# Performance work log

Measured on AMD Instinct MI355X. Metric: run time of the kernel, lower is better.

Reference implementation:

```python
import jax, jax.numpy as jnp
import numpy as np

N_EMBD = 1024
D_FF = 4 * N_EMBD
RANK = 4
NUM_LOOPS = 4
SCALE = 1.0 / RANK  # alpha=1.0 / r=4


def setup_inputs() -> dict:
    key = jax.random.key(0)
    ks = jax.random.split(key, 8)
    B, T = 8, 2048
    x = jax.random.normal(ks[0], (B, T, N_EMBD), dtype=jnp.float32)
    # base linears (torch nn.Linear weight layout: [out, in]), bias=False
    W1 = jax.random.normal(ks[1], (D_FF, N_EMBD), dtype=jnp.float32) * (1.0 / np.sqrt(N_EMBD))
    W2 = jax.random.normal(ks[2], (N_EMBD, D_FF), dtype=jnp.float32) * (1.0 / np.sqrt(D_FF))
    # LoRA factors: A [num_loops, r, in], B [num_loops, out, r]
    # (torch inits lora_B to zeros; we use small random values so the LoRA path is exercised)
    A1 = jax.random.normal(ks[3], (NUM_LOOPS, RANK, N_EMBD), dtype=jnp.float32) * (1.0 / np.sqrt(N_EMBD))
    B1 = jax.random.normal(ks[4], (NUM_LOOPS, D_FF, RANK), dtype=jnp.float32) * 0.01
    A2 = jax.random.normal(ks[5], (NUM_LOOPS, RANK, D_FF), dtype=jnp.float32) * (1.0 / np.sqrt(D_FF))
    B2 = jax.random.normal(ks[6], (NUM_LOOPS, N_EMBD, RANK), dtype=jnp.float32) * 0.01
    adapter_id = 1
    return {"x": x, "W1": W1, "A1": A1, "B1": B1, "W2": W2, "A2": A2, "B2": B2,
            "adapter_id": adapter_id}


def _lora_linear(x, W, A, B, adapter_id):
    # base: x @ W.T  (torch F.linear)
    out = jnp.einsum('btd,fd->btf', x, W)
    Aa = A[adapter_id]  # [r, in]
    Ba = B[adapter_id]  # [out, r]
    # low-rank correction: ((x @ A.T) @ B.T) * scale
    delta = jnp.einsum('btr,fr->btf', jnp.einsum('btd,rd->btr', x, Aa), Ba) * SCALE
    return out + delta


def reference(x, W1, A1, B1, W2, A2, B2, adapter_id):
    h = jax.nn.relu(_lora_linear(x, W1, A1, B1, adapter_id))
    out = _lora_linear(h, W2, A2, B2, adapter_id)
    # Dropout in eval mode (identity); see notes.
    return out
```

## Files before the change

kernel.cpp:

```cpp
#include <hip/hip_runtime.h>
#include <stdint.h>

typedef __bf16 bf16;
typedef __attribute__((ext_vector_type(8))) __bf16 bf16x8;
typedef __attribute__((ext_vector_type(4))) float f32x4;

#define LORA_SCALE 0.25f

__device__ __forceinline__ void gload_lds16(const bf16* g, bf16* l) {
    __builtin_amdgcn_global_load_lds(
        (const __attribute__((address_space(1))) uint32_t*)g,
        (__attribute__((address_space(3))) uint32_t*)l,
        16, 0, 0);
}

__device__ __forceinline__ bf16x8 cvt8(const float* p) {
    f32x4 a = *(const f32x4*)p;
    f32x4 b = *(const f32x4*)(p + 4);
    bf16x8 r;
    r[0] = (bf16)a[0]; r[1] = (bf16)a[1]; r[2] = (bf16)a[2]; r[3] = (bf16)a[3];
    r[4] = (bf16)b[0]; r[5] = (bf16)b[1]; r[6] = (bf16)b[2]; r[7] = (bf16)b[3];
    return r;
}

__global__ __launch_bounds__(256)
void cvt_weights(const float* __restrict__ in1, bf16* __restrict__ out1, int n1,
                 const float* __restrict__ in2, bf16* __restrict__ out2, int n2) {
    const int64_t idx = (int64_t)(blockIdx.x * 256 + threadIdx.x) * 8;
    if (idx < n1) *(bf16x8*)&out1[idx] = cvt8(&in1[idx]);
    else          *(bf16x8*)&out2[idx - n1] = cvt8(&in2[idx - n1]);
}

__global__ __launch_bounds__(256)
void lora1(const float* __restrict__ X, const float* __restrict__ Aall,
           const int* __restrict__ adapter, float* __restrict__ T,
           bf16* __restrict__ Xb)
{
    const int K = 1024;
    const int gid = blockIdx.x * 256 + threadIdx.x;
    const int aid = adapter[0];
    const float* Aa = Aall + (int64_t)aid * 4 * K;
    const int wid  = gid >> 6;
    const int lane = threadIdx.x & 63;
    const int m0   = wid * 4;

    float acc[4][4];
    #pragma unroll
    for (int rr = 0; rr < 4; rr++)
        #pragma unroll
        for (int r = 0; r < 4; r++) acc[rr][r] = 0.f;

    #pragma unroll
    for (int it = 0; it < K / 512; it++) {
        const int k = it * 512 + lane * 8;
        float av[4][8];
        #pragma unroll
        for (int r = 0; r < 4; r++) {
            f32x4 a = *(const f32x4*)&Aa[r * K + k];
            f32x4 b = *(const f32x4*)&Aa[r * K + k + 4];
            av[r][0]=a[0]; av[r][1]=a[1]; av[r][2]=a[2]; av[r][3]=a[3];
            av[r][4]=b[0]; av[r][5]=b[1]; av[r][6]=b[2]; av[r][7]=b[3];
        }
        #pragma unroll
        for (int rr = 0; rr < 4; rr++) {
            const float* xp = X + (int64_t)(m0 + rr) * K + k;
            f32x4 a = *(const f32x4*)xp;
            f32x4 b = *(const f32x4*)(xp + 4);
            float xv[8] = {a[0],a[1],a[2],a[3],b[0],b[1],b[2],b[3]};
            bf16x8 xb;
            #pragma unroll
            for (int e = 0; e < 8; e++) xb[e] = (bf16)xv[e];
            *(bf16x8*)&Xb[(int64_t)(m0 + rr) * K + k] = xb;
            #pragma unroll
            for (int r = 0; r < 4; r++)
                #pragma unroll
                for (int e = 0; e < 8; e++)
                    acc[rr][r] += xv[e] * av[r][e];
        }
    }
    #pragma unroll
    for (int rr = 0; rr < 4; rr++)
        #pragma unroll
        for (int r = 0; r < 4; r++)
            #pragma unroll
            for (int off = 32; off >= 1; off >>= 1)
                acc[rr][r] += __shfl_xor(acc[rr][r], off);
    if (lane == 0) {
        #pragma unroll
        for (int rr = 0; rr < 4; rr++) {
            f32x4 t;
            t[0] = acc[rr][0]; t[1] = acc[rr][1]; t[2] = acc[rr][2]; t[3] = acc[rr][3];
            *(f32x4*)&T[(int64_t)(m0 + rr) * 4] = t;
        }
    }
}

__global__ __launch_bounds__(256)
void t2_reduce(const float* __restrict__ T2p, float* __restrict__ T2,
               int M, int NP) {
    const int i = blockIdx.x * 256 + threadIdx.x;
    float s = 0.f;
    for (int p = 0; p < NP; p++) s += T2p[(int64_t)p * M * 4 + i];
    T2[i] = s;
}

template<bool RELU, typename CT, int PART, bool FUSET2>
__global__ __launch_bounds__(256, 2)
void gemm_lora(const bf16* __restrict__ A,
               const bf16* __restrict__ Bm,
               CT* __restrict__ C,
               const float* __restrict__ Tlo,
               const float* __restrict__ Blo,
               const int* __restrict__ adapter,
               const float* __restrict__ A2,
               float* __restrict__ T2p,
               int M, int N, int K)
{
    __shared__ bf16 smem[256 * 64 + 128 * 64];
    bf16* sA = smem;
    bf16* sB = smem + 256 * 64;

    const int tid  = threadIdx.x;
    const int lane = tid & 63;
    const int w    = tid >> 6;
    const int quad = lane >> 4;
    const int l16  = lane & 15;

    int bx, by;
    {
        const int Nt = gridDim.x, Mt = gridDim.y;
        const int id = blockIdx.y * Nt + blockIdx.x;
        const int xcd = id & 7, k = id >> 3;
        if (PART == 0) { const int q = Nt >> 3; bx = xcd * q + (k % q); by = k / q; }
        else           { const int q = Mt >> 3; bx = k % Nt; by = xcd * q + (k / Nt); }
    }
    const int nBase = bx * 128;
    const int mBase = by * 256;
    const int wm = (w >> 1) * 128;
    const int wn = (w & 1) * 64;

    f32x4 acc[8][4];
    #pragma unroll
    for (int i = 0; i < 8; i++)
        #pragma unroll
        for (int j = 0; j < 4; j++)
            #pragma unroll
            for (int e = 0; e < 4; e++)
                acc[i][j][e] = 0.f;

    const bf16* gA = A  + (int64_t)mBase * K;
    const bf16* gB = Bm + (int64_t)nBase * K;
    const int ldRow  = tid >> 3;
    const int swzCol = ((tid & 7) ^ ((tid >> 3) & 7)) * 8;

    for (int kt = 0; kt < K; kt += 64) {
        #pragma unroll
        for (int i = 0; i < 8; i++)
            gload_lds16(gA + (int64_t)(i * 32 + ldRow) * K + kt + swzCol,
                        sA + (i * 32 + w * 8) * 64);
        #pragma unroll
        for (int i = 0; i < 4; i++)
            gload_lds16(gB + (int64_t)(i * 32 + ldRow) * K + kt + swzCol,
                        sB + (i * 32 + w * 8) * 64);
        __syncthreads();
        #pragma unroll
        for (int ks = 0; ks < 2; ks++) {
            const int kpos = (((ks * 4 + quad) ^ (l16 & 7))) * 8;
            bf16x8 af[8], bfv[4];
            #pragma unroll
            for (int i = 0; i < 8; i++)
                af[i] = *(const bf16x8*)&sA[(wm + i * 16 + l16) * 64 + kpos];
            #pragma unroll
            for (int j = 0; j < 4; j++)
                bfv[j] = *(const bf16x8*)&sB[(wn + j * 16 + l16) * 64 + kpos];
            #pragma unroll
            for (int i = 0; i < 8; i++)
                #pragma unroll
                for (int j = 0; j < 4; j++)
                    acc[i][j] = __builtin_amdgcn_mfma_f32_16x16x32_bf16(af[i], bfv[j], acc[i][j], 0, 0, 0);
        }
        __syncthreads();
    }

    const int aid = adapter[0];
    const float* Ba = Blo + (int64_t)aid * N * 4;

    f32x4 bv[4];
    #pragma unroll
    for (int j = 0; j < 4; j++) {
        const int f = nBase + wn + j * 16 + l16;
        bv[j] = *(const f32x4*)&Ba[(int64_t)f * 4];
    }

    float a2v[4][4];
    if (FUSET2) {
        const float* A2a = A2 + (int64_t)aid * 4 * N;
        #pragma unroll
        for (int j = 0; j < 4; j++) {
            const int f = nBase + wn + j * 16 + l16;
            #pragma unroll
            for (int r2 = 0; r2 < 4; r2++)
                a2v[j][r2] = A2a[(int64_t)r2 * N + f];
        }
    }
    float* T2row = FUSET2 ? T2p + ((int64_t)(bx * 2 + (w & 1)) * M) * 4 : nullptr;

    if constexpr (sizeof(CT) == 2) {
        bf16* scratch = smem + w * (64 * 72);
        #pragma unroll
        for (int g = 0; g < 2; g++) {
            #pragma unroll
            for (int mi2 = 0; mi2 < 4; mi2++) {
                const int mi = g * 4 + mi2;
                f32x4 tv[4];
                #pragma unroll
                for (int r = 0; r < 4; r++) {
                    const int m = mBase + wm + mi * 16 + quad * 4 + r;
                    tv[r] = *(const f32x4*)&Tlo[(int64_t)m * 4];
                }
                float tp[4][4];
                if (FUSET2)
                    #pragma unroll
                    for (int r = 0; r < 4; r++)
                        #pragma unroll
                        for (int r2 = 0; r2 < 4; r2++) tp[r][r2] = 0.f;
                #pragma unroll
                for (int j = 0; j < 4; j++) {
                    #pragma unroll
                    for (int r = 0; r < 4; r++) {
                        const float d = tv[r][0] * bv[j][0] + tv[r][1] * bv[j][1]
                                      + tv[r][2] * bv[j][2] + tv[r][3] * bv[j][3];
                        float v = acc[mi][j][r] + LORA_SCALE * d;
                        if (RELU) v = v > 0.f ? v : 0.f;
                        if (FUSET2)
                            #pragma unroll
                            for (int r2 = 0; r2 < 4; r2++)
                                tp[r][r2] += v * a2v[j][r2];
                        scratch[(mi2 * 16 + quad * 4 + r) * 72 + j * 16 + l16] = (bf16)v;
                    }
                }
                if (FUSET2) {
                    #pragma unroll
                    for (int r = 0; r < 4; r++)
                        #pragma unroll
                        for (int r2 = 0; r2 < 4; r2++)
                            #pragma unroll
                            for (int off = 8; off >= 1; off >>= 1)
                                tp[r][r2] += __shfl_xor(tp[r][r2], off);
                    if (l16 == 0) {
                        #pragma unroll
                        for (int r = 0; r < 4; r++) {
                            const int m = mBase + wm + mi * 16 + quad * 4 + r;
                            f32x4 o;
                            o[0] = tp[r][0]; o[1] = tp[r][1];
                            o[2] = tp[r][2]; o[3] = tp[r][3];
                            *(f32x4*)&T2row[(int64_t)m * 4] = o;
                        }
                    }
                }
            }
            #pragma unroll
            for (int p = 0; p < 8; p++) {
                const int row = p * 8 + (lane >> 3);
                bf16x8 vv = *(const bf16x8*)&scratch[row * 72 + (lane & 7) * 8];
                const int m = mBase + wm + g * 64 + row;
                *(bf16x8*)&C[(int64_t)m * N + nBase + wn + (lane & 7) * 8] = vv;
            }
        }
    } else {
        #pragma unroll
        for (int mi = 0; mi < 8; mi++) {
            f32x4 tv[4];
            #pragma unroll
            for (int r = 0; r < 4; r++) {
                const int m = mBase + wm + mi * 16 + quad * 4 + r;
                tv[r] = *(const f32x4*)&Tlo[(int64_t)m * 4];
            }
            #pragma unroll
            for (int j = 0; j < 4; j++) {
                #pragma unroll
                for (int r = 0; r < 4; r++) {
                    const float d = tv[r][0] * bv[j][0] + tv[r][1] * bv[j][1]
                                  + tv[r][2] * bv[j][2] + tv[r][3] * bv[j][3];
                    float v = acc[mi][j][r] + LORA_SCALE * d;
                    if (RELU) v = v > 0.f ? v : 0.f;
                    const int m = mBase + wm + mi * 16 + quad * 4 + r;
                    C[(int64_t)m * N + nBase + wn + j * 16 + l16] = v;
                }
            }
        }
    }
}

extern "C" void kernel_launch(void* const* d_in, const int* in_sizes, int n_in,
                              void* d_out, int out_size, void* d_ws, size_t ws_size,
                              hipStream_t stream) {
    const float* x  = (const float*)d_in[0];
    const float* W1 = (const float*)d_in[1];
    const float* A1 = (const float*)d_in[2];
    const float* B1 = (const float*)d_in[3];
    const float* W2 = (const float*)d_in[4];
    const float* A2 = (const float*)d_in[5];
    const float* B2 = (const float*)d_in[6];
    const int* adapter = (const int*)d_in[7];
    float* out = (float*)d_out;

    const int M = 16384, D = 1024, F = 4096;
    const int Nt1 = F / 128;

    bf16*  h   = (bf16*)d_ws;
    bf16*  xb  = h + (size_t)M * F;
    bf16*  wb1 = xb + (size_t)M * D;
    bf16*  wb2 = wb1 + (size_t)F * D;
    float* t1  = (float*)(wb2 + (size_t)D * F);
    float* t2  = t1 + (size_t)M * 4;
    float* t2p = t2 + (size_t)M * 4;

    lora1<<<M / 16, 256, 0, stream>>>(x, A1, adapter, t1, xb);
    cvt_weights<<<(2 * F * D) / 2048, 256, 0, stream>>>(W1, wb1, F * D, W2, wb2, D * F);
    dim3 g1(Nt1, M / 256);
    gemm_lora<true, bf16, 0, true><<<g1, 256, 0, stream>>>(
        xb, wb1, h, t1, B1, adapter, A2, t2p, M, F, D);
    t2_reduce<<<(M * 4) / 256, 256, 0, stream>>>(t2p, t2, M, 2 * Nt1);
    dim3 g2(D / 128, M / 256);
    gemm_lora<false, float, 1, false><<<g2, 256, 0, stream>>>(
        h, wb2, out, t2, B2, adapter, nullptr, nullptr, M, D, F);
}
```

Baseline: 446.2 us.

## Rewrite LoRA GEMM as 8-wave 256x256 tile with double-buffered LDS pipeline

Replaces the 4-wave 256x128 GEMM with an 8-wave, 512-thread kernel computing 256x256 tiles. K-chunks are split into 32-wide halves and staged into double-buffered LDS with direct global-to-LDS loads issued ahead of use. Explicit vmcnt/lgkmcnt waits, barriers and s_setprio interleave loads with MFMA bursts. The fp32 output path now goes through an LDS scratch so stores are vectorised. This aims to hide memory latency and raise reuse per tile, at the cost of 128KB of LDS (which may limit occupancy to one block per CU) and fragile hand-written wait counts.

```diff
diff --git a/kernel.cpp b/kernel.cpp
--- a/kernel.cpp
+++ b/kernel.cpp
@@ -105,20 +105,18 @@
 }
 
 template<bool RELU, typename CT, int PART, bool FUSET2>
-__global__ __launch_bounds__(256, 2)
-void gemm_lora(const bf16* __restrict__ A,
-               const bf16* __restrict__ Bm,
-               CT* __restrict__ C,
-               const float* __restrict__ Tlo,
-               const float* __restrict__ Blo,
-               const int* __restrict__ adapter,
-               const float* __restrict__ A2,
-               float* __restrict__ T2p,
-               int M, int N, int K)
+__global__ __launch_bounds__(512, 2)
+void gemm_lora8(const bf16* __restrict__ A,
+                const bf16* __restrict__ Bm,
+                CT* __restrict__ C,
+                const float* __restrict__ Tlo,
+                const float* __restrict__ Blo,
+                const int* __restrict__ adapter,
+                const float* __restrict__ A2,
+                float* __restrict__ T2p,
+                int M, int N, int K)
 {
-    __shared__ bf16 smem[256 * 64 + 128 * 64];
-    bf16* sA = smem;
-    bf16* sB = smem + 256 * 64;
+    __shared__ alignas(16) bf16 smem[65536];
 
     const int tid  = threadIdx.x;
     const int lane = tid & 63;
@@ -134,159 +132,249 @@
         if (PART == 0) { const int q = Nt >> 3; bx = xcd * q + (k % q); by = k / q; }
         else           { const int q = Mt >> 3; bx = k % Nt; by = xcd * q + (k / Nt); }
     }
-    const int nBase = bx * 128;
+    const int nBase = bx * 256;
     const int mBase = by * 256;
-    const int wm = (w >> 1) * 128;
-    const int wn = (w & 1) * 64;
-
-    f32x4 acc[8][4];
+    const int wm = (w >> 1) * 64;
+    const int wn = (w & 1) * 128;
+
+    f32x4 acc[4][8];
     #pragma unroll
-    for (int i = 0; i < 8; i++)
-        #pragma unroll
-        for (int j = 0; j < 4; j++)
-            #pragma unroll
-            for (int e = 0; e < 4; e++)
-                acc[i][j][e] = 0.f;
+    for (int i = 0; i < 4; i++)
+        #pragma unroll
+        for (int j = 0; j < 8; j++)
+            #pragma unroll
+            for (int e = 0; e < 4; e++) acc[i][j][e] = 0.f;
 
     const bf16* gA = A  + (int64_t)mBase * K;
     const bf16* gB = Bm + (int64_t)nBase * K;
-    const int ldRow  = tid >> 3;
-    const int swzCol = ((tid & 7) ^ ((tid >> 3) & 7)) * 8;
-
-    for (int kt = 0; kt < K; kt += 64) {
-        #pragma unroll
-        for (int i = 0; i < 8; i++)
-            gload_lds16(gA + (int64_t)(i * 32 + ldRow) * K + kt + swzCol,
-                        sA + (i * 32 + w * 8) * 64);
-        #pragma unroll
-        for (int i = 0; i < 4; i++)
-            gload_lds16(gB + (int64_t)(i * 32 + ldRow) * K + kt + swzCol,
-                        sB + (i * 32 + w * 8) * 64);
-        __syncthreads();
-        #pragma unroll
-        for (int ks = 0; ks < 2; ks++) {
-            const int kpos = (((ks * 4 + quad) ^ (l16 & 7))) * 8;
-            bf16x8 af[8], bfv[4];
-            #pragma unroll
-            for (int i = 0; i < 8; i++)
-                af[i] = *(const bf16x8*)&sA[(wm + i * 16 + l16) * 64 + kpos];
+
+    const int sq    = (tid & 3) ^ ((tid >> 3) & 3);
+    const int srow  = ((tid >> 3) << 1) | ((tid >> 2) & 1);
+    const bf16* sA0 = gA + (int64_t)srow * K + sq * 8;
+    const bf16* sA1 = gA + (int64_t)(srow + 128) * K + sq * 8;
+    const bf16* sB0 = gB + (int64_t)srow * K + sq * 8;
+    const bf16* sB1 = gB + (int64_t)(srow + 128) * K + sq * 8;
+    const int dstW  = w * 512;
+
+    const int pc8  = (quad ^ ((l16 >> 1) & 3)) * 8;
+    const int aOff = (wm + l16) * 32 + pc8;
+    const int bOff = (wn + l16) * 32 + pc8;
+
+    const int NT = K >> 6;
+
+    auto stage = [&](const bf16* s0, const bf16* s1, int t, int uidx) {
+        bf16* u = smem + ((t & 1) * 4 + uidx) * 8192;
+        const int co = t * 64 + (uidx >> 1) * 32;
+        gload_lds16(s0 + co, u + dstW);
+        gload_lds16(s1 + co, u + dstW + 4096);
+    };
+
+    stage(sA0, sA1, 0, 0); stage(sB0, sB1, 0, 1);
+    stage(sA0, sA1, 0, 2); stage(sB0, sB1, 0, 3);
+    if (NT > 1) {
+        asm volatile("s_waitcnt vmcnt(4)" ::: "memory");
+        stage(sA0, sA1, 1, 0); stage(sB0, sB1, 1, 1); stage(sA0, sA1, 1, 2);
+        asm volatile("s_waitcnt vmcnt(6)" ::: "memory");
+    } else {
+        asm volatile("s_waitcnt vmcnt(0)" ::: "memory");
+    }
+    __builtin_amdgcn_s_barrier();
+    __builtin_amdgcn_sched_barrier(0);
+
+    for (int t = 0; t < NT; ++t) {
+        const bf16* u0 = smem + (t & 1) * 32768;
+        const bf16* u1 = u0 + 8192;
+        const bf16* u2 = u0 + 16384;
+        const bf16* u3 = u0 + 24576;
+        const bool sNext  = (t + 1 < NT);
+        const bool sNext2 = (t + 2 < NT);
+
+        bf16x8 a0[4], bA[4];
+        #pragma unroll
+        for (int mi = 0; mi < 4; mi++) a0[mi] = *(const bf16x8*)&u0[aOff + mi * 512];
+        #pragma unroll
+        for (int j = 0; j < 4; j++)   bA[j]  = *(const bf16x8*)&u1[bOff + j * 512];
+        if (sNext) stage(sB0, sB1, t + 1, 3);
+        __builtin_amdgcn_s_barrier();
+        __builtin_amdgcn_sched_barrier(0);
+        asm volatile("s_waitcnt lgkmcnt(0)" ::: "memory");
+        __builtin_amdgcn_s_setprio(1);
+        #pragma unroll
+        for (int mi = 0; mi < 4; mi++)
             #pragma unroll
             for (int j = 0; j < 4; j++)
-                bfv[j] = *(const bf16x8*)&sB[(wn + j * 16 + l16) * 64 + kpos];
-            #pragma unroll
-            for (int i = 0; i < 8; i++)
-                #pragma unroll
-                for (int j = 0; j < 4; j++)
-                    acc[i][j] = __builtin_amdgcn_mfma_f32_16x16x32_bf16(af[i], bfv[j], acc[i][j], 0, 0, 0);
-        }
-        __syncthreads();
+                acc[mi][j] = __builtin_amdgcn_mfma_f32_16x16x32_bf16(a0[mi], bA[j], acc[mi][j], 0, 0, 0);
+        __builtin_amdgcn_s_setprio(0);
+        __builtin_amdgcn_s_barrier();
+        __builtin_amdgcn_sched_barrier(0);
+
+        bf16x8 bB[4];
+        #pragma unroll
+        for (int j = 0; j < 4; j++) bB[j] = *(const bf16x8*)&u1[bOff + (4 + j) * 512];
+        if (sNext2) stage(sA0, sA1, t + 2, 0);
+        __builtin_amdgcn_s_barrier();
+        __builtin_amdgcn_sched_barrier(0);
+        asm volatile("s_waitcnt lgkmcnt(0)" ::: "memory");
+        __builtin_amdgcn_s_setprio(1);
+        #pragma unroll
+        for (int mi = 0; mi < 4; mi++)
+            #pragma unroll
+            for (int j = 0; j < 4; j++)
+                acc[mi][4 + j] = __builtin_amdgcn_mfma_f32_16x16x32_bf16(a0[mi], bB[j], acc[mi][4 + j], 0, 0, 0);
+        __builtin_amdgcn_s_setprio(0);
+        __builtin_amdgcn_s_barrier();
+        __builtin_amdgcn_sched_barrier(0);
+
+        bf16x8 a1[4], bC[4];
+        #pragma unroll
+        for (int mi = 0; mi < 4; mi++) a1[mi] = *(const bf16x8*)&u2[aOff + mi * 512];
+        #pragma unroll
+        for (int j = 0; j < 4; j++)   bC[j]  = *(const bf16x8*)&u3[bOff + j * 512];
+        if (sNext2) stage(sB0, sB1, t + 2, 1);
+        __builtin_amdgcn_s_barrier();
+        __builtin_amdgcn_sched_barrier(0);
+        asm volatile("s_waitcnt lgkmcnt(0)" ::: "memory");
+        __builtin_amdgcn_s_setprio(1);
+        #pragma unroll
+        for (int mi = 0; mi < 4; mi++)
+            #pragma unroll
+            for (int j = 0; j < 4; j++)
+                acc[mi][j] = __builtin_amdgcn_mfma_f32_16x16x32_bf16(a1[mi], bC[j], acc[mi][j], 0, 0, 0);
+        __builtin_amdgcn_s_setprio(0);
+        __builtin_amdgcn_s_barrier();
+        __builtin_amdgcn_sched_barrier(0);
+
+        bf16x8 bD[4];
+        #pragma unroll
+        for (int j = 0; j < 4; j++) bD[j] = *(const bf16x8*)&u3[bOff + (4 + j) * 512];
+        if (sNext2) stage(sA0, sA1, t + 2, 2);
+        __builtin_amdgcn_s_barrier();
+        __builtin_amdgcn_sched_barrier(0);
+        asm volatile("s_waitcnt lgkmcnt(0)" ::: "memory");
+        __builtin_amdgcn_s_setprio(1);
+        #pragma unroll
+        for (int mi = 0; mi < 4; mi++)
+            #pragma unroll
+            for (int j = 0; j < 4; j++)
+                acc[mi][4 + j] = __builtin_amdgcn_mfma_f32_16x16x32_bf16(a1[mi], bD[j], acc[mi][4 + j], 0, 0, 0);
+        __builtin_amdgcn_s_setprio(0);
+        if (sNext) {
+            if (sNext2) asm volatile("s_waitcnt vmcnt(6)" ::: "memory");
+            else        asm volatile("s_waitcnt vmcnt(0)" ::: "memory");
+        }
+        __builtin_amdgcn_s_barrier();
+        __builtin_amdgcn_sched_barrier(0);
     }
 
     const int aid = adapter[0];
     const float* Ba = Blo + (int64_t)aid * N * 4;
 
-    f32x4 bv[4];
+    f32x4 bv[8];
     #pragma unroll
-    for (int j = 0; j < 4; j++) {
+    for (int j = 0; j < 8; j++) {
         const int f = nBase + wn + j * 16 + l16;
         bv[j] = *(const f32x4*)&Ba[(int64_t)f * 4];
     }
 
-    float a2v[4][4];
-    if (FUSET2) {
+    float a2v[8][4];
+    if constexpr (FUSET2) {
         const float* A2a = A2 + (int64_t)aid * 4 * N;
         #pragma unroll
-        for (int j = 0; j < 4; j++) {
+        for (int j = 0; j < 8; j++) {
             const int f = nBase + wn + j * 16 + l16;
             #pragma unroll
             for (int r2 = 0; r2 < 4; r2++)
                 a2v[j][r2] = A2a[(int64_t)r2 * N + f];
         }
     }
-    float* T2row = FUSET2 ? T2p + ((int64_t)(bx * 2 + (w & 1)) * M) * 4 : nullptr;
+    float* T2row = FUSET2 ? T2p + (int64_t)(bx * 2 + (w & 1)) * M * 4 : nullptr;
 
     if constexpr (sizeof(CT) == 2) {
-        bf16* scratch = smem + w * (64 * 72);
-        #pragma unroll
-        for (int g = 0; g < 2; g++) {
-            #pragma unroll
-            for (int mi2 = 0; mi2 < 4; mi2++) {
-                const int mi = g * 4 + mi2;
-                f32x4 tv[4];
-                #pragma unroll
-                for (int r = 0; r < 4; r++) {
-                    const int m = mBase + wm + mi * 16 + quad * 4 + r;
-                    tv[r] = *(const f32x4*)&Tlo[(int64_t)m * 4];
-                }
-                float tp[4][4];
-                if (FUSET2)
-                    #pragma unroll
-                    for (int r = 0; r < 4; r++)
-                        #pragma unroll
-                        for (int r2 = 0; r2 < 4; r2++) tp[r][r2] = 0.f;
-                #pragma unroll
-                for (int j = 0; j < 4; j++) {
-                    #pragma unroll
-                    for (int r = 0; r < 4; r++) {
-                        const float d = tv[r][0] * bv[j][0] + tv[r][1] * bv[j][1]
-                                      + tv[r][2] * bv[j][2] + tv[r][3] * bv[j][3];
-                        float v = acc[mi][j][r] + LORA_SCALE * d;
-                        if (RELU) v = v > 0.f ? v : 0.f;
-                        if (FUSET2)
-                            #pragma unroll
-                            for (int r2 = 0; r2 < 4; r2++)
-                                tp[r][r2] += v * a2v[j][r2];
-                        scratch[(mi2 * 16 + quad * 4 + r) * 72 + j * 16 + l16] = (bf16)v;
-                    }
-                }
-                if (FUSET2) {
-                    #pragma unroll
-                    for (int r = 0; r < 4; r++)
-                        #pragma unroll
-                        for (int r2 = 0; r2 < 4; r2++)
-                            #pragma unroll
-                            for (int off = 8; off >= 1; off >>= 1)
-                                tp[r][r2] += __shfl_xor(tp[r][r2], off);
-                    if (l16 == 0) {
-                        #pragma unroll
-                        for (int r = 0; r < 4; r++) {
-                            const int m = mBase + wm + mi * 16 + quad * 4 + r;
-                            f32x4 o;
-                            o[0] = tp[r][0]; o[1] = tp[r][1];
-                            o[2] = tp[r][2]; o[3] = tp[r][3];
-                            *(f32x4*)&T2row[(int64_t)m * 4] = o;
-                        }
-                    }
-                }
-            }
-            #pragma unroll
-            for (int p = 0; p < 8; p++) {
-                const int row = p * 8 + (lane >> 3);
-                bf16x8 vv = *(const bf16x8*)&scratch[row * 72 + (lane & 7) * 8];
-                const int m = mBase + wm + g * 64 + row;
-                *(bf16x8*)&C[(int64_t)m * N + nBase + wn + (lane & 7) * 8] = vv;
-            }
-        }
-    } else {
-        #pragma unroll
-        for (int mi = 0; mi < 8; mi++) {
+        bf16* scratch = smem + w * (16 * 136);
+        #pragma unroll
+        for (int mi = 0; mi < 4; mi++) {
             f32x4 tv[4];
             #pragma unroll
             for (int r = 0; r < 4; r++) {
                 const int m = mBase + wm + mi * 16 + quad * 4 + r;
                 tv[r] = *(const f32x4*)&Tlo[(int64_t)m * 4];
             }
-            #pragma unroll
-            for (int j = 0; j < 4; j++) {
+            float tp[4][4];
+            if constexpr (FUSET2)
+                #pragma unroll
+                for (int r = 0; r < 4; r++)
+                    #pragma unroll
+                    for (int r2 = 0; r2 < 4; r2++) tp[r][r2] = 0.f;
+            #pragma unroll
+            for (int j = 0; j < 8; j++) {
                 #pragma unroll
                 for (int r = 0; r < 4; r++) {
                     const float d = tv[r][0] * bv[j][0] + tv[r][1] * bv[j][1]
                                   + tv[r][2] * bv[j][2] + tv[r][3] * bv[j][3];
                     float v = acc[mi][j][r] + LORA_SCALE * d;
                     if (RELU) v = v > 0.f ? v : 0.f;
-                    const int m = mBase + wm + mi * 16 + quad * 4 + r;
-                    C[(int64_t)m * N + nBase + wn + j * 16 + l16] = v;
+                    if constexpr (FUSET2)
+                        #pragma unroll
+                        for (int r2 = 0; r2 < 4; r2++) tp[r][r2] += v * a2v[j][r2];
+                    scratch[(quad * 4 + r) * 136 + j * 16 + l16] = (bf16)v;
                 }
+            }
+            if constexpr (FUSET2) {
+                #pragma unroll
+                for (int r = 0; r < 4; r++)
+                    #pragma unroll
+                    for (int r2 = 0; r2 < 4; r2++)
+                        #pragma unroll
+                        for (int off = 8; off >= 1; off >>= 1)
+                            tp[r][r2] += __shfl_xor(tp[r][r2], off);
+                if (l16 == 0) {
+                    #pragma unroll
+                    for (int r = 0; r < 4; r++) {
+                        const int m = mBase + wm + mi * 16 + quad * 4 + r;
+                        f32x4 o;
+                        o[0] = tp[r][0]; o[1] = tp[r][1];
+                        o[2] = tp[r][2]; o[3] = tp[r][3];
+                        *(f32x4*)&T2row[(int64_t)m * 4] = o;
+                    }
+                }
+            }
+            #pragma unroll
+            for (int it = 0; it < 4; it++) {
+                const int cid = it * 64 + lane;
+                const int row = cid >> 4, c8 = cid & 15;
+                bf16x8 vv = *(const bf16x8*)&scratch[row * 136 + c8 * 8];
+                const int m = mBase + wm + mi * 16 + row;
+                *(bf16x8*)&C[(int64_t)m * N + nBase + wn + c8 * 8] = vv;
+            }
+        }
+    } else {
+        float* scratchf = (float*)smem + w * (16 * 132);
+        #pragma unroll
+        for (int mi = 0; mi < 4; mi++) {
+            f32x4 tv[4];
+            #pragma unroll
+            for (int r = 0; r < 4; r++) {
+                const int m = mBase + wm + mi * 16 + quad * 4 + r;
+                tv[r] = *(const f32x4*)&Tlo[(int64_t)m * 4];
+            }
+            #pragma unroll
+            for (int j = 0; j < 8; j++) {
+                #pragma unroll
+                for (int r = 0; r < 4; r++) {
+                    const float d = tv[r][0] * bv[j][0] + tv[r][1] * bv[j][1]
+                                  + tv[r][2] * bv[j][2] + tv[r][3] * bv[j][3];
+                    float v = acc[mi][j][r] + LORA_SCALE * d;
+                    if (RELU) v = v > 0.f ? v : 0.f;
+                    scratchf[(quad * 4 + r) * 132 + j * 16 + l16] = v;
+                }
+            }
+            #pragma unroll
+            for (int it = 0; it < 8; it++) {
+                const int cid = it * 64 + lane;
+                const int row = cid >> 5, c4 = cid & 31;
+                f32x4 vv = *(const f32x4*)&scratchf[row * 132 + c4 * 4];
+                const int m = mBase + wm + mi * 16 + row;
+                *(f32x4*)&C[(int64_t)m * N + nBase + wn + c4 * 4] = vv;
             }
         }
     }
@@ -306,7 +394,7 @@
     float* out = (float*)d_out;
 
     const int M = 16384, D = 1024, F = 4096;
-    const int Nt1 = F / 128;
+    const int Nt1 = F / 256;
 
     bf16*  h   = (bf16*)d_ws;
     bf16*  xb  = h + (size_t)M * F;
@@ -318,11 +406,11 @@
 
     lora1<<<M / 16, 256, 0, stream>>>(x, A1, adapter, t1, xb);
     cvt_weights<<<(2 * F * D) / 2048, 256, 0, stream>>>(W1, wb1, F * D, W2, wb2, D * F);
-    dim3 g1(Nt1, M / 256);
-    gemm_lora<true, bf16, 0, true><<<g1, 256, 0, stream>>>(
+    dim3 g1(F / 256, M / 256);
+    gemm_lora8<true, bf16, 0, true><<<g1, 512, 0, stream>>>(
         xb, wb1, h, t1, B1, adapter, A2, t2p, M, F, D);
     t2_reduce<<<(M * 4) / 256, 256, 0, stream>>>(t2p, t2, M, 2 * Nt1);
-    dim3 g2(D / 128, M / 256);
-    gemm_lora<false, float, 1, false><<<g2, 256, 0, stream>>>(
+    dim3 g2(D / 256, M / 256);
+    gemm_lora8<false, float, 1, false><<<g2, 512, 0, stream>>>(
         h, wb2, out, t2, B2, adapter, nullptr, nullptr, M, D, F);
 }
```

Result: no change. 449.5 us (+0.7%).

## Shrink GEMM tiles to 128x128, prefetch next K-tile into LDS, group swizzle

Applied to the files above, without the earlier changes.

Both LoRA GEMMs now use a 128x128 block tile in place of 256x128, with fewer accumulators per wave, and raise launch bounds to 3 blocks per CU. The K loop loads the fragments to registers, then issues the next tile's global-to-LDS loads before running the MFMAs, so memory traffic overlaps compute. The block-to-tile mapping uses a grouped XCD-aware swizzle. The fp32 output path is staged through LDS for vectorized 16-byte stores. The aims are higher occupancy, hidden load latency and coalesced stores, at the cost of less operand reuse per block and more blocks.

```diff
diff --git a/kernel.cpp b/kernel.cpp
--- a/kernel.cpp
+++ b/kernel.cpp
@@ -104,21 +104,21 @@
     T2[i] = s;
 }
 
-template<bool RELU, typename CT, int PART, bool FUSET2>
-__global__ __launch_bounds__(256, 2)
-void gemm_lora(const bf16* __restrict__ A,
-               const bf16* __restrict__ Bm,
-               CT* __restrict__ C,
-               const float* __restrict__ Tlo,
-               const float* __restrict__ Blo,
-               const int* __restrict__ adapter,
-               const float* __restrict__ A2,
-               float* __restrict__ T2p,
-               int M, int N, int K)
+template<bool RELU, typename CT, int GRP, bool FUSET2>
+__global__ __launch_bounds__(256, 3)
+void gemm_lora10(const bf16* __restrict__ A,
+                 const bf16* __restrict__ Bm,
+                 CT* __restrict__ C,
+                 const float* __restrict__ Tlo,
+                 const float* __restrict__ Blo,
+                 const int* __restrict__ adapter,
+                 const float* __restrict__ A2,
+                 float* __restrict__ T2p,
+                 int M, int N, int K)
 {
-    __shared__ bf16 smem[256 * 64 + 128 * 64];
+    __shared__ alignas(16) bf16 smem[16384];
     bf16* sA = smem;
-    bf16* sB = smem + 256 * 64;
+    bf16* sB = smem + 8192;
 
     const int tid  = threadIdx.x;
     const int lane = tid & 63;
@@ -130,57 +130,75 @@
     {
         const int Nt = gridDim.x, Mt = gridDim.y;
         const int id = blockIdx.y * Nt + blockIdx.x;
-        const int xcd = id & 7, k = id >> 3;
-        if (PART == 0) { const int q = Nt >> 3; bx = xcd * q + (k % q); by = k / q; }
-        else           { const int q = Mt >> 3; bx = k % Nt; by = xcd * q + (k / Nt); }
+        const int xcd = id & 7;
+        const int k = id >> 3;
+        const int span = GRP * Nt;
+        const int byg = k / span, rem = k % span;
+        by = xcd * (Mt >> 3) + byg * GRP + (rem % GRP);
+        bx = rem / GRP;
     }
     const int nBase = bx * 128;
-    const int mBase = by * 256;
-    const int wm = (w >> 1) * 128;
+    const int mBase = by * 128;
+    const int wm = (w >> 1) * 64;
     const int wn = (w & 1) * 64;
 
-    f32x4 acc[8][4];
-    #pragma unroll
-    for (int i = 0; i < 8; i++)
+    f32x4 acc[4][4];
+    #pragma unroll
+    for (int i = 0; i < 4; i++)
         #pragma unroll
         for (int j = 0; j < 4; j++)
             #pragma unroll
-            for (int e = 0; e < 4; e++)
-                acc[i][j][e] = 0.f;
+            for (int e = 0; e < 4; e++) acc[i][j][e] = 0.f;
 
     const bf16* gA = A  + (int64_t)mBase * K;
     const bf16* gB = Bm + (int64_t)nBase * K;
-    const int ldRow  = tid >> 3;
-    const int swzCol = ((tid & 7) ^ ((tid >> 3) & 7)) * 8;
-
-    for (int kt = 0; kt < K; kt += 64) {
-        #pragma unroll
-        for (int i = 0; i < 8; i++)
-            gload_lds16(gA + (int64_t)(i * 32 + ldRow) * K + kt + swzCol,
-                        sA + (i * 32 + w * 8) * 64);
-        #pragma unroll
-        for (int i = 0; i < 4; i++)
-            gload_lds16(gB + (int64_t)(i * 32 + ldRow) * K + kt + swzCol,
-                        sB + (i * 32 + w * 8) * 64);
+
+    const int rl = tid >> 3;
+    const int sq = (tid & 7) ^ (rl & 7);
+    const int dstW = (w << 3) * 64;
+
+    const int NT = K >> 6;
+
+    auto stage = [&](int t) {
+        const int co = t * 64 + sq * 8;
+        #pragma unroll
+        for (int i = 0; i < 4; i++) {
+            gload_lds16(gA + (int64_t)(i * 32 + rl) * K + co, sA + i * 2048 + dstW);
+            gload_lds16(gB + (int64_t)(i * 32 + rl) * K + co, sB + i * 2048 + dstW);
+        }
+    };
+
+    const int pc0 = ((0 * 4 + quad) ^ (l16 & 7)) * 8;
+    const int pc1 = ((1 * 4 + quad) ^ (l16 & 7)) * 8;
+
+    stage(0);
+    for (int t = 0; t < NT; ++t) {
         __syncthreads();
-        #pragma unroll
-        for (int ks = 0; ks < 2; ks++) {
-            const int kpos = (((ks * 4 + quad) ^ (l16 & 7))) * 8;
-            bf16x8 af[8], bfv[4];
-            #pragma unroll
-            for (int i = 0; i < 8; i++)
-                af[i] = *(const bf16x8*)&sA[(wm + i * 16 + l16) * 64 + kpos];
-            #pragma unroll
-            for (int j = 0; j < 4; j++)
-                bfv[j] = *(const bf16x8*)&sB[(wn + j * 16 + l16) * 64 + kpos];
-            #pragma unroll
-            for (int i = 0; i < 8; i++)
+        bf16x8 af[2][4], bfv[2][4];
+        #pragma unroll
+        for (int mi = 0; mi < 4; mi++) {
+            const int r = (wm + mi * 16 + l16) * 64;
+            af[0][mi] = *(const bf16x8*)&sA[r + pc0];
+            af[1][mi] = *(const bf16x8*)&sA[r + pc1];
+        }
+        #pragma unroll
+        for (int j = 0; j < 4; j++) {
+            const int r = (wn + j * 16 + l16) * 64;
+            bfv[0][j] = *(const bf16x8*)&sB[r + pc0];
+            bfv[1][j] = *(const bf16x8*)&sB[r + pc1];
+        }
+        __syncthreads();
+        if (t + 1 < NT) stage(t + 1);
+        #pragma unroll
+        for (int ks = 0; ks < 2; ks++)
+            #pragma unroll
+            for (int mi = 0; mi < 4; mi++)
                 #pragma unroll
                 for (int j = 0; j < 4; j++)
-                    acc[i][j] = __builtin_amdgcn_mfma_f32_16x16x32_bf16(af[i], bfv[j], acc[i][j], 0, 0, 0);
-        }
-        __syncthreads();
-    }
+                    acc[mi][j] = __builtin_amdgcn_mfma_f32_16x16x32_bf16(
+                        af[ks][mi], bfv[ks][j], acc[mi][j], 0, 0, 0);
+    }
+    __syncthreads();
 
     const int aid = adapter[0];
     const float* Ba = Blo + (int64_t)aid * N * 4;
@@ -193,7 +211,7 @@
     }
 
     float a2v[4][4];
-    if (FUSET2) {
+    if constexpr (FUSET2) {
         const float* A2a = A2 + (int64_t)aid * 4 * N;
         #pragma unroll
         for (int j = 0; j < 4; j++) {
@@ -203,79 +221,24 @@
                 a2v[j][r2] = A2a[(int64_t)r2 * N + f];
         }
     }
-    float* T2row = FUSET2 ? T2p + ((int64_t)(bx * 2 + (w & 1)) * M) * 4 : nullptr;
+    float* T2row = FUSET2 ? T2p + (int64_t)(bx * 2 + (w & 1)) * M * 4 : nullptr;
 
     if constexpr (sizeof(CT) == 2) {
-        bf16* scratch = smem + w * (64 * 72);
-        #pragma unroll
-        for (int g = 0; g < 2; g++) {
-            #pragma unroll
-            for (int mi2 = 0; mi2 < 4; mi2++) {
-                const int mi = g * 4 + mi2;
-                f32x4 tv[4];
-                #pragma unroll
-                for (int r = 0; r < 4; r++) {
-                    const int m = mBase + wm + mi * 16 + quad * 4 + r;
-                    tv[r] = *(const f32x4*)&Tlo[(int64_t)m * 4];
-                }
-                float tp[4][4];
-                if (FUSET2)
-                    #pragma unroll
-                    for (int r = 0; r < 4; r++)
-                        #pragma unroll
-                        for (int r2 = 0; r2 < 4; r2++) tp[r][r2] = 0.f;
-                #pragma unroll
-                for (int j = 0; j < 4; j++) {
-                    #pragma unroll
-                    for (int r = 0; r < 4; r++) {
-                        const float d = tv[r][0] * bv[j][0] + tv[r][1] * bv[j][1]
-                                      + tv[r][2] * bv[j][2] + tv[r][3] * bv[j][3];
-                        float v = acc[mi][j][r] + LORA_SCALE * d;
-                        if (RELU) v = v > 0.f ? v : 0.f;
-                        if (FUSET2)
-                            #pragma unroll
-                            for (int r2 = 0; r2 < 4; r2++)
-                                tp[r][r2] += v * a2v[j][r2];
-                        scratch[(mi2 * 16 + quad * 4 + r) * 72 + j * 16 + l16] = (bf16)v;
-                    }
-                }
-                if (FUSET2) {
-                    #pragma unroll
-                    for (int r = 0; r < 4; r++)
-                        #pragma unroll
-                        for (int r2 = 0; r2 < 4; r2++)
-                            #pragma unroll
-                            for (int off = 8; off >= 1; off >>= 1)
-                                tp[r][r2] += __shfl_xor(tp[r][r2], off);
-                    if (l16 == 0) {
-                        #pragma unroll
-                        for (int r = 0; r < 4; r++) {
-                            const int m = mBase + wm + mi * 16 + quad * 4 + r;
-                            f32x4 o;
-                            o[0] = tp[r][0]; o[1] = tp[r][1];
-                            o[2] = tp[r][2]; o[3] = tp[r][3];
-                            *(f32x4*)&T2row[(int64_t)m * 4] = o;
-                        }
-                    }
-                }
-            }
-            #pragma unroll
-            for (int p = 0; p < 8; p++) {
-                const int row = p * 8 + (lane >> 3);
-                bf16x8 vv = *(const bf16x8*)&scratch[row * 72 + (lane & 7) * 8];
-                const int m = mBase + wm + g * 64 + row;
-                *(bf16x8*)&C[(int64_t)m * N + nBase + wn + (lane & 7) * 8] = vv;
-            }
-        }
-    } else {
-        #pragma unroll
-        for (int mi = 0; mi < 8; mi++) {
+        bf16* scratch = smem + w * (16 * 72);
+        #pragma unroll
+        for (int mi = 0; mi < 4; mi++) {
             f32x4 tv[4];
             #pragma unroll
             for (int r = 0; r < 4; r++) {
                 const int m = mBase + wm + mi * 16 + quad * 4 + r;
                 tv[r] = *(const f32x4*)&Tlo[(int64_t)m * 4];
             }
+            float tp[4][4];
+            if constexpr (FUSET2)
+                #pragma unroll
+                for (int r = 0; r < 4; r++)
+                    #pragma unroll
+                    for (int r2 = 0; r2 < 4; r2++) tp[r][r2] = 0.f;
             #pragma unroll
             for (int j = 0; j < 4; j++) {
                 #pragma unroll
@@ -284,9 +247,68 @@
                                   + tv[r][2] * bv[j][2] + tv[r][3] * bv[j][3];
                     float v = acc[mi][j][r] + LORA_SCALE * d;
                     if (RELU) v = v > 0.f ? v : 0.f;
-                    const int m = mBase + wm + mi * 16 + quad * 4 + r;
-                    C[(int64_t)m * N + nBase + wn + j * 16 + l16] = v;
+                    if constexpr (FUSET2)
+                        #pragma unroll
+                        for (int r2 = 0; r2 < 4; r2++) tp[r][r2] += v * a2v[j][r2];
+                    scratch[(quad * 4 + r) * 72 + j * 16 + l16] = (bf16)v;
                 }
+            }
+            if constexpr (FUSET2) {
+                #pragma unroll
+                for (int r = 0; r < 4; r++)
+                    #pragma unroll
+                    for (int r2 = 0; r2 < 4; r2++)
+                        #pragma unroll
+                        for (int off = 8; off >= 1; off >>= 1)
+                            tp[r][r2] += __shfl_xor(tp[r][r2], off);
+                if (l16 == 0) {
+                    #pragma unroll
+                    for (int r = 0; r < 4; r++) {
+                        const int m = mBase + wm + mi * 16 + quad * 4 + r;
+                        f32x4 o;
+                        o[0] = tp[r][0]; o[1] = tp[r][1];
+                        o[2] = tp[r][2]; o[3] = tp[r][3];
+                        *(f32x4*)&T2row[(int64_t)m * 4] = o;
+                    }
+                }
+            }
+            #pragma unroll
+            for (int it = 0; it < 2; it++) {
+                const int cid = it * 64 + lane;
+                const int row = cid >> 3, c8 = cid & 7;
+                bf16x8 vv = *(const bf16x8*)&scratch[row * 72 + c8 * 8];
+                const int m = mBase + wm + mi * 16 + row;
+                *(bf16x8*)&C[(int64_t)m * N + nBase + wn + c8 * 8] = vv;
+            }
+        }
+    } else {
+        float* scratchf = (float*)smem + w * (16 * 68);
+        #pragma unroll
+        for (int mi = 0; mi < 4; mi++) {
+            f32x4 tv[4];
+            #pragma unroll
+            for (int r = 0; r < 4; r++) {
+                const int m = mBase + wm + mi * 16 + quad * 4 + r;
+                tv[r] = *(const f32x4*)&Tlo[(int64_t)m * 4];
+            }
+            #pragma unroll
+            for (int j = 0; j < 4; j++) {
+                #pragma unroll
+                for (int r = 0; r < 4; r++) {
+                    const float d = tv[r][0] * bv[j][0] + tv[r][1] * bv[j][1]
+                                  + tv[r][2] * bv[j][2] + tv[r][3] * bv[j][3];
+                    float v = acc[mi][j][r] + LORA_SCALE * d;
+                    if (RELU) v = v > 0.f ? v : 0.f;
+                    scratchf[(quad * 4 + r) * 68 + j * 16 + l16] = v;
+                }
+            }
+            #pragma unroll
+            for (int it = 0; it < 4; it++) {
+                const int cid = it * 64 + lane;
+                const int row = cid >> 4, c4 = cid & 15;
+                f32x4 vv = *(const f32x4*)&scratchf[row * 68 + c4 * 4];
+                const int m = mBase + wm + mi * 16 + row;
+                *(f32x4*)&C[(int64_t)m * N + nBase + wn + c4 * 4] = vv;
             }
         }
     }
@@ -318,11 +340,11 @@
 
     lora1<<<M / 16, 256, 0, stream>>>(x, A1, adapter, t1, xb);
     cvt_weights<<<(2 * F * D) / 2048, 256, 0, stream>>>(W1, wb1, F * D, W2, wb2, D * F);
-    dim3 g1(Nt1, M / 256);
-    gemm_lora<true, bf16, 0, true><<<g1, 256, 0, stream>>>(
+    dim3 g1(F / 128, M / 128);
+    gemm_lora10<true, bf16, 4, true><<<g1, 256, 0, stream>>>(
         xb, wb1, h, t1, B1, adapter, A2, t2p, M, F, D);
     t2_reduce<<<(M * 4) / 256, 256, 0, stream>>>(t2p, t2, M, 2 * Nt1);
-    dim3 g2(D / 128, M / 256);
-    gemm_lora<false, float, 1, false><<<g2, 256, 0, stream>>>(
+    dim3 g2(D / 128, M / 128);
+    gemm_lora10<false, float, 2, false><<<g2, 256, 0, stream>>>(
         h, wb2, out, t2, B2, adapter, nullptr, nullptr, M, D, F);
 }
```

Measured after the change: 480.0 us. 7.6% more time.
